# Optimization experiments

Measured on AMD Instinct MI355X. Metric: run time of the kernel, lower is better.

Reference implementation:

```python
import jax, jax.numpy as jnp
import numpy as np

N_IN, N_H, N_OUT = 256, 2048, 256
BATCH, T = 64, 512


def setup_inputs() -> dict:
    key = jax.random.key(0)
    k_u, k_uh, k_hh, k_hy, k_h0 = jax.random.split(key, 5)
    u = jax.random.normal(k_u, (BATCH, T, N_IN), dtype=jnp.float32)
    # sparse_normal_weights with p=1: N(0, g^2/N_src), returned transposed -> (N_src, N_dst)
    W_uh = jax.random.normal(k_uh, (N_IN, N_H), dtype=jnp.float32) / np.sqrt(N_IN)
    W_hh = jax.random.normal(k_hh, (N_H, N_H), dtype=jnp.float32) / np.sqrt(N_H)
    W_hy = jax.random.normal(k_hy, (N_H, N_OUT), dtype=jnp.float32) / np.sqrt(N_H)
    b_h = jnp.zeros((N_H,), dtype=jnp.float32)
    b_y = jnp.zeros((N_OUT,), dtype=jnp.float32)
    # h0 ~ Uniform[-1, 1] (tanh branch)
    h0 = jax.random.uniform(k_h0, (N_H,), dtype=jnp.float32, minval=-1.0, maxval=1.0)
    tau = jnp.ones((N_H,), dtype=jnp.float32)
    return {"u": u, "W_uh": W_uh, "W_hh": W_hh, "W_hy": W_hy,
            "b_h": b_h, "b_y": b_y, "h0": h0, "tau": tau}


def reference(u, W_uh, W_hh, W_hy, b_h, b_y, h0, tau):
    # Leaky CTRNN, f_h=tanh, f_out=softmax, noise=0.0, h0=None path
    alpha = 1.0 / tau                      # (N_h,)
    h0c = jnp.clip(h0, -1.0, 1.0)          # clip_initial_state for tanh
    batch = u.shape[0]
    h_init = jnp.broadcast_to(h0c, (batch, N_H))

    def step(h, u_t):
        pre = h @ W_hh + u_t @ W_uh + b_h          # (B, N_h)
        h_new = (1.0 - alpha) * h + alpha * jnp.tanh(pre)
        y_t = jax.nn.softmax(h_new @ W_hy + b_y, axis=1)  # (B, N_out)
        return h_new, y_t

    u_t_first = jnp.swapaxes(u, 0, 1)              # (T, B, N_in)
    _, y = jax.lax.scan(step, h_init, u_t_first)   # y: (T, B, N_out)
    return jnp.swapaxes(y, 0, 1)                   # (B, T, N_out)
```

## Files before the change

### kernel.cpp

```cpp
#include <hip/hip_runtime.h>
#include <hip/hip_fp16.h>

#define N_INP 256
#define NH    2048
#define NOUT  256
#define BB    64
#define TT    512
#define GRIDN 128
#define NWAVE (GRIDN * 4)

typedef __bf16 bf16x8 __attribute__((ext_vector_type(8)));
typedef float  f32x4  __attribute__((ext_vector_type(4)));

__device__ __forceinline__ unsigned short f2bf(float f) {
  unsigned u = __float_as_uint(f);
  u += 0x7fffu + ((u >> 16) & 1u);
  return (unsigned short)(u >> 16);
}

__device__ __forceinline__ float fast_tanh(float x) {
  x = fminf(9.0f, fmaxf(-9.0f, x));
  float e = __expf(2.0f * x);
  return (e - 1.0f) / (e + 1.0f);
}

__device__ __forceinline__ f32x4 mfma16(uint4 a, uint4 b, f32x4 c) {
  return __builtin_amdgcn_mfma_f32_16x16x32_bf16(
      __builtin_bit_cast(bf16x8, a), __builtin_bit_cast(bf16x8, b), c, 0, 0, 0);
}

__global__ void k_zero(unsigned* __restrict__ p, int n) {
  int i = blockIdx.x * 256 + threadIdx.x;
  if (i < n) p[i] = 0;
}

__global__ void k_ut(const float* __restrict__ u, unsigned short* __restrict__ ut) {
  int idx = blockIdx.x * 256 + threadIdx.x;
  int k4 = idx & 63;
  int rowbt = idx >> 6;
  int t = rowbt >> 6, b = rowbt & 63;
  float4 f = *(const float4*)(u + ((size_t)b * TT + t) * N_INP + k4 * 4);
  uint2 pk;
  pk.x = f2bf(f.x) | ((unsigned)f2bf(f.y) << 16);
  pk.y = f2bf(f.z) | ((unsigned)f2bf(f.w) << 16);
  *(uint2*)(ut + (size_t)rowbt * N_INP + k4 * 4) = pk;
}

__global__ void k_swz(const float* __restrict__ W, unsigned short* __restrict__ Wf, int N) {
  int lane = threadIdx.x;
  int nt16 = N >> 4;
  int kb = blockIdx.x / nt16;
  int nt = blockIdx.x - kb * nt16;
  int k0 = kb * 32 + ((lane >> 4) << 3);
  int c  = nt * 16 + (lane & 15);
  unsigned short v[8];
#pragma unroll
  for (int j = 0; j < 8; ++j) v[j] = f2bf(W[(size_t)(k0 + j) * N + c]);
  uint4 p;
  p.x = v[0] | ((unsigned)v[1] << 16);
  p.y = v[2] | ((unsigned)v[3] << 16);
  p.z = v[4] | ((unsigned)v[5] << 16);
  p.w = v[6] | ((unsigned)v[7] << 16);
  ((uint4*)Wf)[(size_t)blockIdx.x * 64 + lane] = p;
}

__global__ __launch_bounds__(256) void k_step(
    const float* __restrict__ Whh, const float* __restrict__ Wuh,
    const float* __restrict__ b_h, const float* __restrict__ tau,
    const float* __restrict__ h0, const unsigned short* __restrict__ ut,
    unsigned short* __restrict__ H, unsigned* __restrict__ flags) {
  __shared__ unsigned short lds[64 * 64 * 8];
  const int cgp = blockIdx.x;
  const int tid = threadIdx.x;
  const int wave = tid >> 6;
  const int lane = tid & 63;
  const int q = lane >> 4, p = lane & 15;

  for (int s = tid; s < 64 * 64; s += 256) {
    int kb = s >> 6, l = s & 63;
    int k0 = kb * 32 + ((l >> 4) << 3);
    int c = cgp * 16 + (l & 15);
    unsigned short v[8];
#pragma unroll
    for (int j = 0; j < 8; ++j) v[j] = f2bf(Whh[(size_t)(k0 + j) * NH + c]);
    uint4 pk;
    pk.x = v[0] | ((unsigned)v[1] << 16);
    pk.y = v[2] | ((unsigned)v[3] << 16);
    pk.z = v[4] | ((unsigned)v[5] << 16);
    pk.w = v[6] | ((unsigned)v[7] << 16);
    ((uint4*)lds)[s] = pk;
  }

  const int c = cgp * 16 + p;
  const float al = 1.0f / tau[c];
  const float onem = 1.0f - al;
  const float bh_c = b_h[c];
  const float h0c = fminf(1.0f, fmaxf(-1.0f, h0[c]));
  float hprev[4] = {h0c, h0c, h0c, h0c};
  const int rbase = wave * 16;
  const bool even = (p & 1) == 0;
  const int halfc = cgp * 8 + (p >> 1);
  unsigned* H32 = (unsigned*)H;

  uint4 wu[8];
#pragma unroll
  for (int kb = 0; kb < 8; ++kb) {
    unsigned short v[8];
#pragma unroll
    for (int j = 0; j < 8; ++j)
      v[j] = f2bf(Wuh[(size_t)(kb * 32 + q * 8 + j) * NH + c]);
    wu[kb].x = v[0] | ((unsigned)v[1] << 16);
    wu[kb].y = v[2] | ((unsigned)v[3] << 16);
    wu[kb].z = v[4] | ((unsigned)v[5] << 16);
    wu[kb].w = v[6] | ((unsigned)v[7] << 16);
  }

  __syncthreads();

  {
    unsigned mine = f2bf(h0c);
    unsigned other = (unsigned)__shfl_xor((int)mine, 1);
    unsigned pk0 = even ? (mine | (other << 16)) : (other | (mine << 16));
    if (even) {
#pragma unroll
      for (int r = 0; r < 4; ++r)
        __hip_atomic_store(H32 + (size_t)(rbase + q * 4 + r) * (NH / 2) + halfc,
                           pk0, __ATOMIC_RELAXED, __HIP_MEMORY_SCOPE_AGENT);
    }
  }
  __builtin_amdgcn_fence(__ATOMIC_RELEASE, "workgroup");
  if (lane == 0)
    __hip_atomic_store(flags + (size_t)wave * GRIDN + cgp, 1u, __ATOMIC_RELAXED,
                       __HIP_MEMORY_SCOPE_AGENT);

  const uint4* ldsv = (const uint4*)lds;
  f32x4 acc[4];

  for (int t = 0; t < TT; ++t) {
    {
      const uint4* Au = (const uint4*)(ut + ((size_t)t * BB + rbase + p) * N_INP + q * 8);
#pragma unroll
      for (int j = 0; j < 4; ++j) acc[j] = (f32x4){0.f, 0.f, 0.f, 0.f};
#pragma unroll
      for (int kb = 0; kb < 8; ++kb)
        acc[kb & 3] = mfma16(Au[kb * 4], wu[kb], acc[kb & 3]);
    }

    const unsigned* fl = flags + (size_t)t * NWAVE + wave * GRIDN;
    for (;;) {
      unsigned v0 = __hip_atomic_load(fl + lane, __ATOMIC_RELAXED,
                                      __HIP_MEMORY_SCOPE_AGENT);
      unsigned v1 = __hip_atomic_load(fl + 64 + lane, __ATOMIC_RELAXED,
                                      __HIP_MEMORY_SCOPE_AGENT);
      if (__all((v0 != 0u) && (v1 != 0u))) break;
    }
    __builtin_amdgcn_fence(__ATOMIC_ACQUIRE, "workgroup");

    const uint4* Ar = (const uint4*)(H + (size_t)t * BB * NH + (size_t)(rbase + p) * NH + q * 8);
    uint4 a[8];
#pragma unroll
    for (int j = 0; j < 8; ++j) a[j] = Ar[j * 4];
#pragma unroll
    for (int kb = 0; kb < 64; kb += 8) {
      uint4 an[8];
      if (kb < 56) {
#pragma unroll
        for (int j = 0; j < 8; ++j) an[j] = Ar[(kb + 8 + j) * 4];
      }
#pragma unroll
      for (int j = 0; j < 8; ++j)
        acc[j & 3] = mfma16(a[j], ldsv[(kb + j) * 64 + lane], acc[j & 3]);
      if (kb < 56) {
#pragma unroll
        for (int j = 0; j < 8; ++j) a[j] = an[j];
      }
    }

    unsigned* H32n = H32 + (size_t)(t + 1) * BB * (NH / 2);
#pragma unroll
    for (int r = 0; r < 4; ++r) {
      float pre = acc[0][r] + acc[1][r] + acc[2][r] + acc[3][r] + bh_c;
      float hn = onem * hprev[r] + al * fast_tanh(pre);
      hprev[r] = hn;
      unsigned mine = f2bf(hn);
      unsigned other = (unsigned)__shfl_xor((int)mine, 1);
      unsigned pk = even ? (mine | (other << 16)) : (other | (mine << 16));
      if (even)
        __hip_atomic_store(H32n + (size_t)(rbase + q * 4 + r) * (NH / 2) + halfc,
                           pk, __ATOMIC_RELAXED, __HIP_MEMORY_SCOPE_AGENT);
    }

    __builtin_amdgcn_fence(__ATOMIC_RELEASE, "workgroup");
    if (lane == 0)
      __hip_atomic_store(flags + (size_t)(t + 1) * NWAVE + wave * GRIDN + cgp, 1u,
                         __ATOMIC_RELAXED, __HIP_MEMORY_SCOPE_AGENT);
  }
}

__global__ __launch_bounds__(256) void k_y(
    const unsigned short* __restrict__ H, const unsigned short* __restrict__ Wyf,
    const float* __restrict__ b_y, float* __restrict__ out) {
  int wave = threadIdx.x >> 6, lane = threadIdx.x & 63;
  int q = lane >> 4, p = lane & 15;
  int R = blockIdx.x * 64 + wave * 16;
  const uint4* A = (const uint4*)(H + (size_t)(R + BB + p) * NH + q * 8);
  const uint4* Bf = (const uint4*)Wyf;
  f32x4 acc[16];
#pragma unroll
  for (int nt = 0; nt < 16; ++nt) acc[nt] = (f32x4){0.f, 0.f, 0.f, 0.f};
  for (int kb = 0; kb < 64; ++kb) {
    uint4 a = A[kb * 4];
#pragma unroll
    for (int nt = 0; nt < 16; ++nt) {
      uint4 b = Bf[(size_t)(kb * 16 + nt) * 64 + lane];
      acc[nt] = mfma16(a, b, acc[nt]);
    }
  }
  float bb[16];
#pragma unroll
  for (int nt = 0; nt < 16; ++nt) bb[nt] = b_y[nt * 16 + p];
#pragma unroll
  for (int r = 0; r < 4; ++r) {
    int row = R + q * 4 + r;
    int tI = row >> 6, bI = row & 63;
    float lg[16];
    float mx = -1e30f;
#pragma unroll
    for (int nt = 0; nt < 16; ++nt) { lg[nt] = acc[nt][r] + bb[nt]; mx = fmaxf(mx, lg[nt]); }
#pragma unroll
    for (int d = 1; d < 16; d <<= 1) mx = fmaxf(mx, __shfl_xor(mx, d));
    float s = 0.f;
#pragma unroll
    for (int nt = 0; nt < 16; ++nt) { lg[nt] = __expf(lg[nt] - mx); s += lg[nt]; }
#pragma unroll
    for (int d = 1; d < 16; d <<= 1) s += __shfl_xor(s, d);
    float inv = 1.0f / s;
    float* orow = out + ((size_t)bI * TT + tI) * NOUT;
#pragma unroll
    for (int nt = 0; nt < 16; ++nt) orow[nt * 16 + p] = lg[nt] * inv;
  }
}

extern "C" void kernel_launch(void* const* d_in, const int* in_sizes, int n_in,
                              void* d_out, int out_size, void* d_ws, size_t ws_size,
                              hipStream_t stream) {
  (void)in_sizes; (void)n_in; (void)out_size; (void)ws_size;
  const float* u   = (const float*)d_in[0];
  const float* Wuh = (const float*)d_in[1];
  const float* Whh = (const float*)d_in[2];
  const float* Why = (const float*)d_in[3];
  const float* b_h = (const float*)d_in[4];
  const float* b_y = (const float*)d_in[5];
  const float* h0  = (const float*)d_in[6];
  const float* tau = (const float*)d_in[7];
  float* out = (float*)d_out;

  char* ws = (char*)d_ws;
  unsigned short* H = (unsigned short*)ws;
  size_t off = (size_t)(TT + 1) * BB * NH * 2;
  unsigned short* ut = (unsigned short*)(ws + off);
  off += (size_t)TT * BB * N_INP * 2;
  unsigned short* Wyf = (unsigned short*)(ws + off);
  off += (size_t)NH * NOUT * 2;
  unsigned* flags = (unsigned*)(ws + off);

  const int nz = (TT + 1) * NWAVE;
  k_zero<<<dim3((nz + 255) / 256), dim3(256), 0, stream>>>(flags, nz);
  k_ut<<<dim3(8192), dim3(256), 0, stream>>>(u, ut);
  k_swz<<<dim3((NH / 32) * (NOUT / 16)), dim3(64), 0, stream>>>(Why, Wyf, NOUT);

  void* args[] = {(void*)&Whh, (void*)&Wuh, (void*)&b_h, (void*)&tau,
                  (void*)&h0, (void*)&ut, (void*)&H, (void*)&flags};
  hipLaunchCooperativeKernel((const void*)k_step, dim3(GRIDN), dim3(256), args, 0, stream);

  k_y<<<dim3(512), dim3(256), 0, stream>>>(H, Wyf, b_y, out);
}
```

Baseline: 4.886 ms.

## Split recurrent K-dimension across four waves per row block with LDS reduction

Each workgroup grows from 4 to 16 waves. The K dimension of the per-step h@W_hh product is split four ways, so each wave runs 16 MFMAs instead of 64, and the input projection is split the same way. Partial sums are reduced through LDS by the leader wave, which alone polls global flags and publishes the new hidden state. Helper waves wait on a shared-memory counter. This shortens the serial critical path per timestep, at the cost of two __syncthreads per step, extra LDS traffic and intra-workgroup spinning.

```diff
diff --git a/kernel.cpp b/kernel.cpp
--- a/kernel.cpp
+++ b/kernel.cpp
@@ -64,19 +64,23 @@
   ((uint4*)Wf)[(size_t)blockIdx.x * 64 + lane] = p;
 }
 
-__global__ __launch_bounds__(256) void k_step(
+__global__ __launch_bounds__(1024) void k_step(
     const float* __restrict__ Whh, const float* __restrict__ Wuh,
     const float* __restrict__ b_h, const float* __restrict__ tau,
     const float* __restrict__ h0, const unsigned short* __restrict__ ut,
     unsigned short* __restrict__ H, unsigned* __restrict__ flags) {
   __shared__ unsigned short lds[64 * 64 * 8];
+  __shared__ f32x4 ldsP[12 * 64 * 4];
+  __shared__ unsigned bar_cnt[4];
   const int cgp = blockIdx.x;
   const int tid = threadIdx.x;
-  const int wave = tid >> 6;
+  const int wid = tid >> 6;
+  const int w = wid >> 2;
+  const int h = wid & 3;
   const int lane = tid & 63;
   const int q = lane >> 4, p = lane & 15;
 
-  for (int s = tid; s < 64 * 64; s += 256) {
+  for (int s = tid; s < 64 * 64; s += 1024) {
     int kb = s >> 6, l = s & 63;
     int k0 = kb * 32 + ((l >> 4) << 3);
     int c = cgp * 16 + (l & 15);
@@ -90,6 +94,7 @@
     pk.w = v[6] | ((unsigned)v[7] << 16);
     ((uint4*)lds)[s] = pk;
   }
+  if (tid < 4) bar_cnt[tid] = 0;
 
   const int c = cgp * 16 + p;
   const float al = 1.0f / tau[c];
@@ -97,27 +102,28 @@
   const float bh_c = b_h[c];
   const float h0c = fminf(1.0f, fmaxf(-1.0f, h0[c]));
   float hprev[4] = {h0c, h0c, h0c, h0c};
-  const int rbase = wave * 16;
+  const int rbase = w * 16;
   const bool even = (p & 1) == 0;
   const int halfc = cgp * 8 + (p >> 1);
   unsigned* H32 = (unsigned*)H;
 
-  uint4 wu[8];
-#pragma unroll
-  for (int kb = 0; kb < 8; ++kb) {
+  uint4 wu[2];
+#pragma unroll
+  for (int i = 0; i < 2; ++i) {
+    int kbg = 2 * h + i;
     unsigned short v[8];
 #pragma unroll
     for (int j = 0; j < 8; ++j)
-      v[j] = f2bf(Wuh[(size_t)(kb * 32 + q * 8 + j) * NH + c]);
-    wu[kb].x = v[0] | ((unsigned)v[1] << 16);
-    wu[kb].y = v[2] | ((unsigned)v[3] << 16);
-    wu[kb].z = v[4] | ((unsigned)v[5] << 16);
-    wu[kb].w = v[6] | ((unsigned)v[7] << 16);
+      v[j] = f2bf(Wuh[(size_t)(kbg * 32 + q * 8 + j) * NH + c]);
+    wu[i].x = v[0] | ((unsigned)v[1] << 16);
+    wu[i].y = v[2] | ((unsigned)v[3] << 16);
+    wu[i].z = v[4] | ((unsigned)v[5] << 16);
+    wu[i].w = v[6] | ((unsigned)v[7] << 16);
   }
 
   __syncthreads();
 
-  {
+  if (h == 0) {
     unsigned mine = f2bf(h0c);
     unsigned other = (unsigned)__shfl_xor((int)mine, 1);
     unsigned pk0 = even ? (mine | (other << 16)) : (other | (mine << 16));
@@ -127,13 +133,15 @@
         __hip_atomic_store(H32 + (size_t)(rbase + q * 4 + r) * (NH / 2) + halfc,
                            pk0, __ATOMIC_RELAXED, __HIP_MEMORY_SCOPE_AGENT);
     }
-  }
-  __builtin_amdgcn_fence(__ATOMIC_RELEASE, "workgroup");
-  if (lane == 0)
-    __hip_atomic_store(flags + (size_t)wave * GRIDN + cgp, 1u, __ATOMIC_RELAXED,
-                       __HIP_MEMORY_SCOPE_AGENT);
+    __builtin_amdgcn_fence(__ATOMIC_RELEASE, "workgroup");
+    if (lane == 0)
+      __hip_atomic_store(flags + (size_t)w * GRIDN + cgp, 1u, __ATOMIC_RELAXED,
+                         __HIP_MEMORY_SCOPE_AGENT);
+  }
 
   const uint4* ldsv = (const uint4*)lds;
+  const int kb0 = h * 16;
+  const int slot = ((h - 1) * 4 + w) * 256 + lane * 4;
   f32x4 acc[4];
 
   for (int t = 0; t < TT; ++t) {
@@ -142,58 +150,86 @@
 #pragma unroll
       for (int j = 0; j < 4; ++j) acc[j] = (f32x4){0.f, 0.f, 0.f, 0.f};
 #pragma unroll
-      for (int kb = 0; kb < 8; ++kb)
-        acc[kb & 3] = mfma16(Au[kb * 4], wu[kb], acc[kb & 3]);
-    }
-
-    const unsigned* fl = flags + (size_t)t * NWAVE + wave * GRIDN;
-    for (;;) {
-      unsigned v0 = __hip_atomic_load(fl + lane, __ATOMIC_RELAXED,
-                                      __HIP_MEMORY_SCOPE_AGENT);
-      unsigned v1 = __hip_atomic_load(fl + 64 + lane, __ATOMIC_RELAXED,
-                                      __HIP_MEMORY_SCOPE_AGENT);
-      if (__all((v0 != 0u) && (v1 != 0u))) break;
-    }
-    __builtin_amdgcn_fence(__ATOMIC_ACQUIRE, "workgroup");
-
-    const uint4* Ar = (const uint4*)(H + (size_t)t * BB * NH + (size_t)(rbase + p) * NH + q * 8);
-    uint4 a[8];
-#pragma unroll
-    for (int j = 0; j < 8; ++j) a[j] = Ar[j * 4];
-#pragma unroll
-    for (int kb = 0; kb < 64; kb += 8) {
-      uint4 an[8];
-      if (kb < 56) {
-#pragma unroll
-        for (int j = 0; j < 8; ++j) an[j] = Ar[(kb + 8 + j) * 4];
+      for (int i = 0; i < 2; ++i) {
+        int kbg = 2 * h + i;
+        acc[kbg & 3] = mfma16(Au[kbg * 4], wu[i], acc[kbg & 3]);
       }
-#pragma unroll
-      for (int j = 0; j < 8; ++j)
-        acc[j & 3] = mfma16(a[j], ldsv[(kb + j) * 64 + lane], acc[j & 3]);
-      if (kb < 56) {
-#pragma unroll
-        for (int j = 0; j < 8; ++j) a[j] = an[j];
+    }
+
+    if (h == 0) {
+      const unsigned* fl = flags + (size_t)t * NWAVE + w * GRIDN;
+      for (;;) {
+        unsigned v0 = __hip_atomic_load(fl + lane, __ATOMIC_RELAXED,
+                                        __HIP_MEMORY_SCOPE_AGENT);
+        unsigned v1 = __hip_atomic_load(fl + 64 + lane, __ATOMIC_RELAXED,
+                                        __HIP_MEMORY_SCOPE_AGENT);
+        if (__all((v0 != 0u) && (v1 != 0u))) break;
       }
-    }
-
-    unsigned* H32n = H32 + (size_t)(t + 1) * BB * (NH / 2);
-#pragma unroll
-    for (int r = 0; r < 4; ++r) {
-      float pre = acc[0][r] + acc[1][r] + acc[2][r] + acc[3][r] + bh_c;
-      float hn = onem * hprev[r] + al * fast_tanh(pre);
-      hprev[r] = hn;
-      unsigned mine = f2bf(hn);
-      unsigned other = (unsigned)__shfl_xor((int)mine, 1);
-      unsigned pk = even ? (mine | (other << 16)) : (other | (mine << 16));
-      if (even)
-        __hip_atomic_store(H32n + (size_t)(rbase + q * 4 + r) * (NH / 2) + halfc,
-                           pk, __ATOMIC_RELAXED, __HIP_MEMORY_SCOPE_AGENT);
-    }
-
-    __builtin_amdgcn_fence(__ATOMIC_RELEASE, "workgroup");
-    if (lane == 0)
-      __hip_atomic_store(flags + (size_t)(t + 1) * NWAVE + wave * GRIDN + cgp, 1u,
-                         __ATOMIC_RELAXED, __HIP_MEMORY_SCOPE_AGENT);
+      __builtin_amdgcn_fence(__ATOMIC_ACQUIRE, "workgroup");
+      __hip_atomic_store(&bar_cnt[w], (unsigned)(t + 1), __ATOMIC_RELAXED,
+                         __HIP_MEMORY_SCOPE_WORKGROUP);
+    } else {
+      while (__hip_atomic_load(&bar_cnt[w], __ATOMIC_RELAXED,
+                               __HIP_MEMORY_SCOPE_WORKGROUP) < (unsigned)(t + 1))
+        __builtin_amdgcn_s_sleep(1);
+      __builtin_amdgcn_fence(__ATOMIC_ACQUIRE, "workgroup");
+    }
+
+    const uint4* Ar = (const uint4*)(H + (size_t)t * BB * NH +
+                                     (size_t)(rbase + p) * NH + q * 8);
+    uint4 a[8], an[8];
+#pragma unroll
+    for (int j = 0; j < 8; ++j) a[j] = Ar[(kb0 + j) * 4];
+#pragma unroll
+    for (int j = 0; j < 8; ++j) an[j] = Ar[(kb0 + 8 + j) * 4];
+#pragma unroll
+    for (int j = 0; j < 8; ++j)
+      acc[(kb0 + j) & 3] = mfma16(a[j], ldsv[(kb0 + j) * 64 + lane], acc[(kb0 + j) & 3]);
+#pragma unroll
+    for (int j = 0; j < 8; ++j)
+      acc[(kb0 + 8 + j) & 3] =
+          mfma16(an[j], ldsv[(kb0 + 8 + j) * 64 + lane], acc[(kb0 + 8 + j) & 3]);
+
+    if (h != 0) {
+#pragma unroll
+      for (int ci = 0; ci < 4; ++ci) ldsP[slot + ci] = acc[ci];
+    }
+    __syncthreads();
+    f32x4 p1[4], p2[4], p3[4];
+    if (h == 0) {
+#pragma unroll
+      for (int ci = 0; ci < 4; ++ci) {
+        p1[ci] = ldsP[(0 * 4 + w) * 256 + lane * 4 + ci];
+        p2[ci] = ldsP[(1 * 4 + w) * 256 + lane * 4 + ci];
+        p3[ci] = ldsP[(2 * 4 + w) * 256 + lane * 4 + ci];
+      }
+    }
+    __syncthreads();
+
+    if (h == 0) {
+#pragma unroll
+      for (int ci = 0; ci < 4; ++ci)
+        acc[ci] = ((acc[ci] + p1[ci]) + p2[ci]) + p3[ci];
+
+      unsigned* H32n = H32 + (size_t)(t + 1) * BB * (NH / 2);
+#pragma unroll
+      for (int r = 0; r < 4; ++r) {
+        float pre = acc[0][r] + acc[1][r] + acc[2][r] + acc[3][r] + bh_c;
+        float hn = onem * hprev[r] + al * fast_tanh(pre);
+        hprev[r] = hn;
+        unsigned mine = f2bf(hn);
+        unsigned other = (unsigned)__shfl_xor((int)mine, 1);
+        unsigned pk = even ? (mine | (other << 16)) : (other | (mine << 16));
+        if (even)
+          __hip_atomic_store(H32n + (size_t)(rbase + q * 4 + r) * (NH / 2) + halfc,
+                             pk, __ATOMIC_RELAXED, __HIP_MEMORY_SCOPE_AGENT);
+      }
+
+      __builtin_amdgcn_fence(__ATOMIC_RELEASE, "workgroup");
+      if (lane == 0)
+        __hip_atomic_store(flags + (size_t)(t + 1) * NWAVE + w * GRIDN + cgp, 1u,
+                           __ATOMIC_RELAXED, __HIP_MEMORY_SCOPE_AGENT);
+    }
   }
 }
 
@@ -271,7 +307,7 @@
 
   void* args[] = {(void*)&Whh, (void*)&Wuh, (void*)&b_h, (void*)&tau,
                   (void*)&h0, (void*)&ut, (void*)&H, (void*)&flags};
-  hipLaunchCooperativeKernel((const void*)k_step, dim3(GRIDN), dim3(256), args, 0, stream);
+  hipLaunchCooperativeKernel((const void*)k_step, dim3(GRIDN), dim3(1024), args, 0, stream);
 
   k_y<<<dim3(512), dim3(256), 0, stream>>>(H, Wyf, b_y, out);
 }
```

Measured after the change: 8.441 ms. +72.8%, slower.
